# Kernel tuning notes

Hardware: AMD Instinct MI355X
Metric: run time of the kernel (lower is better)

## Reference

```python
import jax, jax.numpy as jnp
import numpy as np


def setup_inputs() -> dict:
    key = jax.random.key(0)
    ks = jax.random.split(key, 10)
    B, T = 64, 2048
    inp_p, inp_q, out = 512, 512, 512
    def xavier(k, shape):
        fan_in, fan_out = shape[1], shape[0]
        limit = np.sqrt(6.0 / (fan_in + fan_out))
        return jax.random.uniform(k, shape, jnp.float32, -limit, limit)
    return {
        "input_p": jax.random.normal(ks[0], (B, inp_p), jnp.float32),
        "input_q": jax.random.normal(ks[1], (B, T, inp_q), jnp.float32),
        "h_tm1": jax.random.normal(ks[2], (B, out), jnp.float32),
        "Wp": xavier(ks[3], (out, inp_p)),
        "bp": jnp.zeros((out,), jnp.float32),
        "Wq": xavier(ks[4], (out, inp_q)),
        "bq": jnp.zeros((out,), jnp.float32),
        "Wr": xavier(ks[5], (out, out)),
        "br": jnp.zeros((out,), jnp.float32),
        "w": 0.05 * jax.random.normal(ks[6], (out,), jnp.float32),
        "match_b": jnp.ones((1,), jnp.float32),
        "depth": 0,
    }


def reference(input_p, input_q, h_tm1, Wp, bp, Wq, bq, Wr, br, w, match_b, depth):
    # depth selects the layer; single layer (depth=0) parameters provided.
    G_p = (input_p @ Wp.T + bp)[:, None, :]          # [B, 1, out]
    G_q = jnp.einsum("btq,oq->bto", input_q, Wq) + bq  # [B, T, out]
    G_r = (h_tm1 @ Wr.T + br)[:, None, :]            # [B, 1, out]
    G = jnp.tanh(G_p + G_q + G_r)                    # [B, T, out]
    alpha = jnp.einsum("bto,o->bt", G, w) + match_b[0]  # [B, T]
    alpha = jax.nn.softmax(alpha, axis=-1)
    z = jnp.einsum("bt,btq->bq", alpha, input_q)     # [B, inp_q]
    return jnp.concatenate([input_p, z], axis=1)     # [B, inp_p+inp_q]
```

## Files before the change

### kernel.cpp

```cpp
#include <hip/hip_runtime.h>
#include <stdint.h>
#include <stddef.h>


typedef __attribute__((ext_vector_type(8))) short short8;
typedef __attribute__((ext_vector_type(8))) unsigned short ushort8v;
typedef __attribute__((ext_vector_type(4))) float f32x4;

__device__ __forceinline__ unsigned short f2bf(float f) {
    unsigned int u = __builtin_bit_cast(unsigned int, f);
    return (unsigned short)((u + 0x7FFFu + ((u >> 16) & 1u)) >> 16);
}

__device__ __forceinline__ void gload_lds16(const void* g, void* l) {
    __builtin_amdgcn_global_load_lds(
        (const __attribute__((address_space(1))) unsigned int*)g,
        (__attribute__((address_space(3))) unsigned int*)l, 16, 0, 0);
}

__global__ __launch_bounds__(256) void k_zero(float* __restrict__ p) {
    int i = (blockIdx.x * 256 + threadIdx.x) * 4;
    *(float4*)(p + i) = make_float4(0.f, 0.f, 0.f, 0.f);
}

__global__ __launch_bounds__(256) void k_convert(const float* __restrict__ Wq,
                                                 unsigned short* __restrict__ Wq_bf) {
    int i = (blockIdx.x * 256 + threadIdx.x) * 8;
    float4 a = *(const float4*)(Wq + i);
    float4 b = *(const float4*)(Wq + i + 4);
    ushort8v o;
    o[0] = f2bf(a.x); o[1] = f2bf(a.y); o[2] = f2bf(a.z); o[3] = f2bf(a.w);
    o[4] = f2bf(b.x); o[5] = f2bf(b.y); o[6] = f2bf(b.z); o[7] = f2bf(b.w);
    *(ushort8v*)(Wq_bf + i) = o;
}

__global__ __launch_bounds__(256) void k_prq(
        const float* __restrict__ ip, const float* __restrict__ h,
        const float* __restrict__ Wp, const float* __restrict__ Wr,
        const float* __restrict__ bp, const float* __restrict__ bq,
        const float* __restrict__ br, float* __restrict__ prq) {
    __shared__ float ip_lds[64][68];
    __shared__ float h_lds[64][68];
    __shared__ float wp_lds[8][68];
    __shared__ float wr_lds[8][68];
    const int tid = threadIdx.x;
    const int o0 = blockIdx.x * 8;
    const int bb = tid >> 3;
    const int oo = tid & 7;
    float acc0 = 0.f, acc1 = 0.f;
    const int lrow = tid >> 2;
    const int lcol = (tid & 3) * 16;
    for (int kc = 0; kc < 512; kc += 64) {
        #pragma unroll
        for (int j = 0; j < 16; j += 4) {
            float4 v = *(const float4*)(ip + lrow * 512 + kc + lcol + j);
            ip_lds[lrow][lcol + j] = v.x; ip_lds[lrow][lcol + j + 1] = v.y;
            ip_lds[lrow][lcol + j + 2] = v.z; ip_lds[lrow][lcol + j + 3] = v.w;
            float4 u = *(const float4*)(h + lrow * 512 + kc + lcol + j);
            h_lds[lrow][lcol + j] = u.x; h_lds[lrow][lcol + j + 1] = u.y;
            h_lds[lrow][lcol + j + 2] = u.z; h_lds[lrow][lcol + j + 3] = u.w;
        }
        if (tid < 128) {
            int r = tid >> 4, c = (tid & 15) * 4;
            float4 v = *(const float4*)(Wp + (size_t)(o0 + r) * 512 + kc + c);
            wp_lds[r][c] = v.x; wp_lds[r][c + 1] = v.y; wp_lds[r][c + 2] = v.z; wp_lds[r][c + 3] = v.w;
        } else {
            int t2 = tid - 128;
            int r = t2 >> 4, c = (t2 & 15) * 4;
            float4 v = *(const float4*)(Wr + (size_t)(o0 + r) * 512 + kc + c);
            wr_lds[r][c] = v.x; wr_lds[r][c + 1] = v.y; wr_lds[r][c + 2] = v.z; wr_lds[r][c + 3] = v.w;
        }
        __syncthreads();
        #pragma unroll 4
        for (int k = 0; k < 64; ++k) {
            float wpv = wp_lds[oo][k], wrv = wr_lds[oo][k];
            acc0 += ip_lds[bb][k] * wpv + h_lds[bb][k] * wrv;
            acc1 += ip_lds[bb + 32][k] * wpv + h_lds[bb + 32][k] * wrv;
        }
        __syncthreads();
    }
    const int o = o0 + oo;
    float base = bp[o] + bq[o] + br[o];
    prq[bb * 512 + o] = acc0 + base;
    prq[(bb + 32) * 512 + o] = acc1 + base;
}

__global__ __launch_bounds__(256, 3) void k_gq(
        const float* __restrict__ iq, const unsigned short* __restrict__ Wq_bf,
        const float* __restrict__ prq, const float* __restrict__ wv,
        float* __restrict__ logits) {
    __shared__ float A_t[128][32];
    __shared__ unsigned short B_t[128][32];
    __shared__ float w_lds[128];
    __shared__ float prq_lds[128];
    __shared__ float red[2][128];

    const int tid = threadIdx.x;
    const int bid = blockIdx.x;
    const int orig = (bid & 7) * 512 + (bid >> 3);
    const int m0 = (orig >> 2) * 128;
    const int n0 = (orig & 3) * 128;
    const int b = m0 >> 11;

    if (tid < 128) {
        w_lds[tid] = wv[n0 + tid];
        prq_lds[tid] = prq[b * 512 + n0 + tid];
    }

    const int lane = tid & 63;
    const int wave = tid >> 6;
    const int wm = wave >> 1;
    const int wn = wave & 1;
    const int r16 = lane & 15;
    const int cc = lane >> 4;

    const int ha0 = (((2 * cc) ^ (r16 & 7)) << 2);
    const int ha1 = (((2 * cc + 1) ^ (r16 & 7)) << 2);
    const int bswz = ((cc ^ ((r16 >> 1) & 3)) << 3);

    const float* asrc[4];
    #pragma unroll
    for (int r = 0; r < 4; ++r) {
        int t = r * 256 + tid;
        int row = t >> 3, s = t & 7;
        asrc[r] = iq + (size_t)(m0 + row) * 512 + ((s ^ (row & 7)) << 2);
    }
    const unsigned short* bsrc[2];
    #pragma unroll
    for (int r = 0; r < 2; ++r) {
        int u = r * 256 + tid;
        int row = u >> 2, s = u & 3;
        bsrc[r] = Wq_bf + (size_t)(n0 + row) * 512 + ((s ^ ((row >> 1) & 3)) << 3);
    }
    char* adst = (char*)A_t + wave * 1024;
    char* bdst = (char*)B_t + wave * 1024;

    f32x4 acc[4][4];
    #pragma unroll
    for (int i = 0; i < 4; ++i)
        #pragma unroll
        for (int j = 0; j < 4; ++j) acc[i][j] = (f32x4){0.f, 0.f, 0.f, 0.f};

    for (int k0 = 0; k0 < 512; k0 += 32) {
        gload_lds16(asrc[0] + k0, adst);
        gload_lds16(asrc[1] + k0, adst + 4096);
        gload_lds16(asrc[2] + k0, adst + 8192);
        gload_lds16(asrc[3] + k0, adst + 12288);
        gload_lds16(bsrc[0] + k0, bdst);
        gload_lds16(bsrc[1] + k0, bdst + 4096);
        __syncthreads();

        short8 af[4];
        #pragma unroll
        for (int mf = 0; mf < 4; ++mf) {
            const float* rp = &A_t[wm * 64 + mf * 16 + r16][0];
            f32x4 x0 = *(const f32x4*)(rp + ha0);
            f32x4 x1 = *(const f32x4*)(rp + ha1);
            ushort8v u;
            u[0] = f2bf(x0[0]); u[1] = f2bf(x0[1]); u[2] = f2bf(x0[2]); u[3] = f2bf(x0[3]);
            u[4] = f2bf(x1[0]); u[5] = f2bf(x1[1]); u[6] = f2bf(x1[2]); u[7] = f2bf(x1[3]);
            af[mf] = __builtin_bit_cast(short8, u);
        }
        #pragma unroll
        for (int nf = 0; nf < 4; ++nf) {
            short8 bfr = *(const short8*)&B_t[wn * 64 + nf * 16 + r16][bswz];
            #pragma unroll
            for (int mf = 0; mf < 4; ++mf)
                acc[mf][nf] = __builtin_amdgcn_mfma_f32_16x16x32_bf16(af[mf], bfr, acc[mf][nf], 0, 0, 0);
        }
        __syncthreads();
    }

    float part[4][4];
    #pragma unroll
    for (int mf = 0; mf < 4; ++mf)
        #pragma unroll
        for (int j = 0; j < 4; ++j) part[mf][j] = 0.f;

    #pragma unroll
    for (int nf = 0; nf < 4; ++nf) {
        int c = wn * 64 + nf * 16 + r16;
        float wc = w_lds[c];
        float pc = prq_lds[c];
        #pragma unroll
        for (int mf = 0; mf < 4; ++mf) {
            #pragma unroll
            for (int j = 0; j < 4; ++j) {
                float x = acc[mf][nf][j] + pc;
                float e = __expf(2.f * x);
                part[mf][j] += wc * (1.f - 2.f / (e + 1.f));
            }
        }
    }
    #pragma unroll
    for (int mf = 0; mf < 4; ++mf)
        #pragma unroll
        for (int j = 0; j < 4; ++j) {
            float v = part[mf][j];
            v += __shfl_xor(v, 1);
            v += __shfl_xor(v, 2);
            v += __shfl_xor(v, 4);
            v += __shfl_xor(v, 8);
            part[mf][j] = v;
        }
    if (r16 == 0) {
        #pragma unroll
        for (int mf = 0; mf < 4; ++mf)
            #pragma unroll
            for (int j = 0; j < 4; ++j)
                red[wn][wm * 64 + mf * 16 + cc * 4 + j] = part[mf][j];
    }
    __syncthreads();
    if (tid < 128)
        atomicAdd(&logits[m0 + tid], red[0][tid] + red[1][tid]);
}

__global__ __launch_bounds__(256) void k_stats(const float* __restrict__ logits,
                                               const float* __restrict__ ip,
                                               float* __restrict__ out,
                                               float* __restrict__ stats) {
    const int b = blockIdx.x, tid = threadIdx.x;
    __shared__ float sm[256];
    float m = -1e30f;
    for (int i = tid; i < 2048; i += 256) m = fmaxf(m, logits[b * 2048 + i]);
    sm[tid] = m;
    __syncthreads();
    for (int s = 128; s > 0; s >>= 1) {
        if (tid < s) sm[tid] = fmaxf(sm[tid], sm[tid + s]);
        __syncthreads();
    }
    float bmax = sm[0];
    __syncthreads();
    float ssum = 0.f;
    for (int i = tid; i < 2048; i += 256) ssum += __expf(logits[b * 2048 + i] - bmax);
    sm[tid] = ssum;
    __syncthreads();
    for (int s = 128; s > 0; s >>= 1) {
        if (tid < s) sm[tid] += sm[tid + s];
        __syncthreads();
    }
    if (tid == 0) { stats[b * 2] = bmax; stats[b * 2 + 1] = sm[0]; }
    out[b * 1024 + tid] = ip[b * 512 + tid];
    out[b * 1024 + 256 + tid] = ip[b * 512 + 256 + tid];
    out[b * 1024 + 512 + tid] = 0.f;
    out[b * 1024 + 768 + tid] = 0.f;
}

#define TC 128
__global__ __launch_bounds__(256) void k_z(const float* __restrict__ logits,
                                           const float* __restrict__ stats,
                                           const float* __restrict__ iq,
                                           float* __restrict__ out) {
    const int blk = blockIdx.x;
    const int b = blk >> 4;
    const int c = blk & 15;
    const int tid = threadIdx.x;
    __shared__ float al[TC];
    const float bmax = stats[b * 2];
    const float inv = 1.f / stats[b * 2 + 1];
    if (tid < TC) al[tid] = __expf(logits[b * 2048 + c * TC + tid] - bmax) * inv;
    __syncthreads();
    const int q = tid * 2;
    float ax = 0.f, ay = 0.f;
    const float* base = iq + ((size_t)b * 2048 + (size_t)c * TC) * 512 + q;
    #pragma unroll 4
    for (int t = 0; t < TC; ++t) {
        float2 v = *(const float2*)(base + (size_t)t * 512);
        float a = al[t];
        ax += a * v.x;
        ay += a * v.y;
    }
    atomicAdd(&out[b * 1024 + 512 + q], ax);
    atomicAdd(&out[b * 1024 + 512 + q + 1], ay);
}

extern "C" void kernel_launch(void* const* d_in, const int* in_sizes, int n_in,
                              void* d_out, int out_size, void* d_ws, size_t ws_size,
                              hipStream_t stream) {
    const float* input_p = (const float*)d_in[0];
    const float* input_q = (const float*)d_in[1];
    const float* h_tm1   = (const float*)d_in[2];
    const float* Wp      = (const float*)d_in[3];
    const float* bp      = (const float*)d_in[4];
    const float* Wq      = (const float*)d_in[5];
    const float* bq      = (const float*)d_in[6];
    const float* Wr      = (const float*)d_in[7];
    const float* br      = (const float*)d_in[8];
    const float* wv      = (const float*)d_in[9];
    float* out = (float*)d_out;

    char* ws = (char*)d_ws;
    unsigned short* Wq_bf = (unsigned short*)ws;
    float* prq    = (float*)(ws + 512 * 1024);
    float* logits = (float*)(ws + 640 * 1024);
    float* stats  = (float*)(ws + 1152 * 1024);

    k_zero<<<dim3(128), dim3(256), 0, stream>>>(logits);
    k_convert<<<dim3(128), dim3(256), 0, stream>>>(Wq, Wq_bf);
    k_prq<<<dim3(64), dim3(256), 0, stream>>>(input_p, h_tm1, Wp, Wr, bp, bq, br, prq);
    k_gq<<<dim3(4096), dim3(256), 0, stream>>>(input_q, Wq_bf, prq, wv, logits);
    k_stats<<<dim3(64), dim3(256), 0, stream>>>(logits, input_p, out, stats);
    k_z<<<dim3(64 * 16), dim3(256), 0, stream>>>(logits, stats, input_q, out);
}
```

Baseline: 219.0 us.

## Prefetch fp32 A tile into registers and store bf16 to LDS

```diff
diff --git a/kernel.cpp b/kernel.cpp
--- a/kernel.cpp
+++ b/kernel.cpp
@@ -1,4 +1,5 @@
 #include <hip/hip_runtime.h>
+#include <hip/hip_bf16.h>
 #include <stdint.h>
 #include <stddef.h>
 
@@ -89,7 +90,7 @@
         const float* __restrict__ iq, const unsigned short* __restrict__ Wq_bf,
         const float* __restrict__ prq, const float* __restrict__ wv,
         float* __restrict__ logits) {
-    __shared__ float A_t[128][32];
+    __shared__ unsigned short A_t[128][32];
     __shared__ unsigned short B_t[128][32];
     __shared__ float w_lds[128];
     __shared__ float prq_lds[128];
@@ -113,18 +114,18 @@
     const int wn = wave & 1;
     const int r16 = lane & 15;
     const int cc = lane >> 4;
-
-    const int ha0 = (((2 * cc) ^ (r16 & 7)) << 2);
-    const int ha1 = (((2 * cc + 1) ^ (r16 & 7)) << 2);
-    const int bswz = ((cc ^ ((r16 >> 1) & 3)) << 3);
-
+    const int swz = ((cc ^ ((r16 >> 1) & 3)) << 3);
+
+    const int g4 = tid & 7;
     const float* asrc[4];
+    unsigned short* adst[4];
     #pragma unroll
     for (int r = 0; r < 4; ++r) {
-        int t = r * 256 + tid;
-        int row = t >> 3, s = t & 7;
-        asrc[r] = iq + (size_t)(m0 + row) * 512 + ((s ^ (row & 7)) << 2);
-    }
+        int arow = r * 32 + (tid >> 3);
+        asrc[r] = iq + (size_t)(m0 + arow) * 512 + g4 * 4;
+        adst[r] = &A_t[arow][(((g4 >> 1) ^ ((arow >> 1) & 3)) << 3) + (g4 & 1) * 4];
+    }
+
     const unsigned short* bsrc[2];
     #pragma unroll
     for (int r = 0; r < 2; ++r) {
@@ -132,7 +133,6 @@
         int row = u >> 2, s = u & 3;
         bsrc[r] = Wq_bf + (size_t)(n0 + row) * 512 + ((s ^ ((row >> 1) & 3)) << 3);
     }
-    char* adst = (char*)A_t + wave * 1024;
     char* bdst = (char*)B_t + wave * 1024;
 
     f32x4 acc[4][4];
@@ -141,35 +141,53 @@
         #pragma unroll
         for (int j = 0; j < 4; ++j) acc[i][j] = (f32x4){0.f, 0.f, 0.f, 0.f};
 
-    for (int k0 = 0; k0 < 512; k0 += 32) {
-        gload_lds16(asrc[0] + k0, adst);
-        gload_lds16(asrc[1] + k0, adst + 4096);
-        gload_lds16(asrc[2] + k0, adst + 8192);
-        gload_lds16(asrc[3] + k0, adst + 12288);
-        gload_lds16(bsrc[0] + k0, bdst);
-        gload_lds16(bsrc[1] + k0, bdst + 4096);
-        __syncthreads();
-
-        short8 af[4];
-        #pragma unroll
-        for (int mf = 0; mf < 4; ++mf) {
-            const float* rp = &A_t[wm * 64 + mf * 16 + r16][0];
-            f32x4 x0 = *(const f32x4*)(rp + ha0);
-            f32x4 x1 = *(const f32x4*)(rp + ha1);
-            ushort8v u;
-            u[0] = f2bf(x0[0]); u[1] = f2bf(x0[1]); u[2] = f2bf(x0[2]); u[3] = f2bf(x0[3]);
-            u[4] = f2bf(x1[0]); u[5] = f2bf(x1[1]); u[6] = f2bf(x1[2]); u[7] = f2bf(x1[3]);
-            af[mf] = __builtin_bit_cast(short8, u);
-        }
-        #pragma unroll
-        for (int nf = 0; nf < 4; ++nf) {
-            short8 bfr = *(const short8*)&B_t[wn * 64 + nf * 16 + r16][bswz];
-            #pragma unroll
-            for (int mf = 0; mf < 4; ++mf)
-                acc[mf][nf] = __builtin_amdgcn_mfma_f32_16x16x32_bf16(af[mf], bfr, acc[mf][nf], 0, 0, 0);
-        }
-        __syncthreads();
-    }
+    float4 rA[4], rB[4];
+
+#define LOADA(RN, K)                                   \
+    RN[0] = *(const float4*)(asrc[0] + (K));           \
+    RN[1] = *(const float4*)(asrc[1] + (K));           \
+    RN[2] = *(const float4*)(asrc[2] + (K));           \
+    RN[3] = *(const float4*)(asrc[3] + (K));
+
+#define CVTW(RC, r)                                                              \
+    {                                                                            \
+        union { __hip_bfloat162 h[2]; uint2 v; } u_;                             \
+        u_.h[0] = __float22bfloat162_rn(make_float2(RC[r].x, RC[r].y));          \
+        u_.h[1] = __float22bfloat162_rn(make_float2(RC[r].z, RC[r].w));          \
+        *(uint2*)adst[r] = u_.v;                                                 \
+    }
+
+#define STEP(K0, RC, RN, KN)                                                     \
+    {                                                                            \
+        __syncthreads();                                                         \
+        CVTW(RC, 0) CVTW(RC, 1) CVTW(RC, 2) CVTW(RC, 3)                          \
+        gload_lds16(bsrc[0] + (K0), bdst);                                       \
+        gload_lds16(bsrc[1] + (K0), bdst + 4096);                                \
+        __syncthreads();                                                         \
+        LOADA(RN, KN);                                                           \
+        short8 af[4];                                                            \
+        af[0] = *(const short8*)&A_t[wm * 64 + 0 * 16 + r16][swz];               \
+        af[1] = *(const short8*)&A_t[wm * 64 + 1 * 16 + r16][swz];               \
+        af[2] = *(const short8*)&A_t[wm * 64 + 2 * 16 + r16][swz];               \
+        af[3] = *(const short8*)&A_t[wm * 64 + 3 * 16 + r16][swz];               \
+        _Pragma("unroll")                                                        \
+        for (int nf = 0; nf < 4; ++nf) {                                         \
+            short8 bfr = *(const short8*)&B_t[wn * 64 + nf * 16 + r16][swz];     \
+            acc[0][nf] = __builtin_amdgcn_mfma_f32_16x16x32_bf16(af[0], bfr, acc[0][nf], 0, 0, 0); \
+            acc[1][nf] = __builtin_amdgcn_mfma_f32_16x16x32_bf16(af[1], bfr, acc[1][nf], 0, 0, 0); \
+            acc[2][nf] = __builtin_amdgcn_mfma_f32_16x16x32_bf16(af[2], bfr, acc[2][nf], 0, 0, 0); \
+            acc[3][nf] = __builtin_amdgcn_mfma_f32_16x16x32_bf16(af[3], bfr, acc[3][nf], 0, 0, 0); \
+        }                                                                        \
+    }
+
+    LOADA(rA, 0);
+    for (int k0 = 0; k0 < 512; k0 += 64) {
+        STEP(k0, rA, rB, k0 + 32);
+        STEP(k0 + 32, rB, rA, (k0 + 64 < 512) ? (k0 + 64) : 480);
+    }
+#undef STEP
+#undef CVTW
+#undef LOADA
 
     float part[4][4];
     #pragma unroll
```

Result: slower. 226.3 us (+3.4%).

## Double-buffer GEMM tiles and convert A to bf16 once during staging

Applied to the files above, without the earlier changes.

```diff
diff --git a/kernel.cpp b/kernel.cpp
--- a/kernel.cpp
+++ b/kernel.cpp
@@ -1,4 +1,5 @@
 #include <hip/hip_runtime.h>
+#include <hip/hip_bf16.h>
 #include <stdint.h>
 #include <stddef.h>
 
@@ -16,6 +17,15 @@
     __builtin_amdgcn_global_load_lds(
         (const __attribute__((address_space(1))) unsigned int*)g,
         (__attribute__((address_space(3))) unsigned int*)l, 16, 0, 0);
+}
+
+__device__ __forceinline__ short8 cvt8(float4 a, float4 b) {
+    union { __hip_bfloat162 h[4]; short8 s; } u;
+    u.h[0] = __float22bfloat162_rn(make_float2(a.x, a.y));
+    u.h[1] = __float22bfloat162_rn(make_float2(a.z, a.w));
+    u.h[2] = __float22bfloat162_rn(make_float2(b.x, b.y));
+    u.h[3] = __float22bfloat162_rn(make_float2(b.z, b.w));
+    return u.s;
 }
 
 __global__ __launch_bounds__(256) void k_zero(float* __restrict__ p) {
@@ -89,8 +99,8 @@
         const float* __restrict__ iq, const unsigned short* __restrict__ Wq_bf,
         const float* __restrict__ prq, const float* __restrict__ wv,
         float* __restrict__ logits) {
-    __shared__ float A_t[128][32];
-    __shared__ unsigned short B_t[128][32];
+    __shared__ unsigned short A2[2][4096];
+    __shared__ unsigned short B2[2][4096];
     __shared__ float w_lds[128];
     __shared__ float prq_lds[128];
     __shared__ float red[2][128];
@@ -113,27 +123,20 @@
     const int wn = wave & 1;
     const int r16 = lane & 15;
     const int cc = lane >> 4;
-
-    const int ha0 = (((2 * cc) ^ (r16 & 7)) << 2);
-    const int ha1 = (((2 * cc + 1) ^ (r16 & 7)) << 2);
-    const int bswz = ((cc ^ ((r16 >> 1) & 3)) << 3);
-
-    const float* asrc[4];
-    #pragma unroll
-    for (int r = 0; r < 4; ++r) {
-        int t = r * 256 + tid;
-        int row = t >> 3, s = t & 7;
-        asrc[r] = iq + (size_t)(m0 + row) * 512 + ((s ^ (row & 7)) << 2);
-    }
-    const unsigned short* bsrc[2];
-    #pragma unroll
-    for (int r = 0; r < 2; ++r) {
-        int u = r * 256 + tid;
-        int row = u >> 2, s = u & 3;
-        bsrc[r] = Wq_bf + (size_t)(n0 + row) * 512 + ((s ^ ((row >> 1) & 3)) << 3);
-    }
-    char* adst = (char*)A_t + wave * 1024;
-    char* bdst = (char*)B_t + wave * 1024;
+    const int swz = ((cc ^ ((r16 >> 1) & 3)) << 3);
+
+    const int ar0 = tid >> 2, ac0 = tid & 3;
+    const int ar1 = 64 + (tid >> 2), ac1 = tid & 3;
+    const float* asrc0 = iq + (size_t)(m0 + ar0) * 512 + ac0 * 8;
+    const float* asrc1 = iq + (size_t)(m0 + ar1) * 512 + ac1 * 8;
+    const int aoff0 = ar0 * 32 + ((ac0 ^ ((ar0 >> 1) & 3)) << 3);
+    const int aoff1 = ar1 * 32 + ((ac1 ^ ((ar1 >> 1) & 3)) << 3);
+
+    const int brw0 = tid >> 2, bs0 = (tid & 3) ^ ((brw0 >> 1) & 3);
+    const int brw1 = 64 + (tid >> 2);
+    const int bs1 = (tid & 3) ^ ((brw1 >> 1) & 3);
+    const unsigned short* bsrc0 = Wq_bf + (size_t)(n0 + brw0) * 512 + (bs0 << 3);
+    const unsigned short* bsrc1 = Wq_bf + (size_t)(n0 + brw1) * 512 + (bs1 << 3);
 
     f32x4 acc[4][4];
     #pragma unroll
@@ -141,35 +144,56 @@
         #pragma unroll
         for (int j = 0; j < 4; ++j) acc[i][j] = (f32x4){0.f, 0.f, 0.f, 0.f};
 
-    for (int k0 = 0; k0 < 512; k0 += 32) {
-        gload_lds16(asrc[0] + k0, adst);
-        gload_lds16(asrc[1] + k0, adst + 4096);
-        gload_lds16(asrc[2] + k0, adst + 8192);
-        gload_lds16(asrc[3] + k0, adst + 12288);
-        gload_lds16(bsrc[0] + k0, bdst);
-        gload_lds16(bsrc[1] + k0, bdst + 4096);
-        __syncthreads();
-
-        short8 af[4];
-        #pragma unroll
-        for (int mf = 0; mf < 4; ++mf) {
-            const float* rp = &A_t[wm * 64 + mf * 16 + r16][0];
-            f32x4 x0 = *(const f32x4*)(rp + ha0);
-            f32x4 x1 = *(const f32x4*)(rp + ha1);
-            ushort8v u;
-            u[0] = f2bf(x0[0]); u[1] = f2bf(x0[1]); u[2] = f2bf(x0[2]); u[3] = f2bf(x0[3]);
-            u[4] = f2bf(x1[0]); u[5] = f2bf(x1[1]); u[6] = f2bf(x1[2]); u[7] = f2bf(x1[3]);
-            af[mf] = __builtin_bit_cast(short8, u);
-        }
-        #pragma unroll
-        for (int nf = 0; nf < 4; ++nf) {
-            short8 bfr = *(const short8*)&B_t[wn * 64 + nf * 16 + r16][bswz];
-            #pragma unroll
-            for (int mf = 0; mf < 4; ++mf)
-                acc[mf][nf] = __builtin_amdgcn_mfma_f32_16x16x32_bf16(af[mf], bfr, acc[mf][nf], 0, 0, 0);
-        }
-        __syncthreads();
-    }
+    float4 ra0, ra1, ra2, ra3;
+
+    gload_lds16(bsrc0, (char*)&B2[0][0] + wave * 1024);
+    gload_lds16(bsrc1, (char*)&B2[0][0] + 4096 + wave * 1024);
+    ra0 = *(const float4*)(asrc0);
+    ra1 = *(const float4*)(asrc0 + 4);
+    ra2 = *(const float4*)(asrc1);
+    ra3 = *(const float4*)(asrc1 + 4);
+    *(short8*)&A2[0][aoff0] = cvt8(ra0, ra1);
+    *(short8*)&A2[0][aoff1] = cvt8(ra2, ra3);
+    asm volatile("s_waitcnt vmcnt(0) lgkmcnt(0)" ::: "memory");
+    __builtin_amdgcn_sched_barrier(0);
+    __builtin_amdgcn_s_barrier();
+
+#define PHASE(K, C, PF)                                                          \
+    {                                                                            \
+        if (PF) {                                                                \
+            gload_lds16(bsrc0 + (K) + 32, (char*)&B2[(C) ^ 1][0] + wave * 1024); \
+            gload_lds16(bsrc1 + (K) + 32, (char*)&B2[(C) ^ 1][0] + 4096 + wave * 1024); \
+            ra0 = *(const float4*)(asrc0 + (K) + 32);                            \
+            ra1 = *(const float4*)(asrc0 + (K) + 36);                            \
+            ra2 = *(const float4*)(asrc1 + (K) + 32);                            \
+            ra3 = *(const float4*)(asrc1 + (K) + 36);                            \
+        }                                                                        \
+        short8 af0 = *(const short8*)&A2[C][(wm * 64 +  0 + r16) * 32 + swz];    \
+        short8 af1 = *(const short8*)&A2[C][(wm * 64 + 16 + r16) * 32 + swz];    \
+        short8 af2 = *(const short8*)&A2[C][(wm * 64 + 32 + r16) * 32 + swz];    \
+        short8 af3 = *(const short8*)&A2[C][(wm * 64 + 48 + r16) * 32 + swz];    \
+        _Pragma("unroll")                                                        \
+        for (int nf = 0; nf < 4; ++nf) {                                         \
+            short8 bfr = *(const short8*)&B2[C][(wn * 64 + nf * 16 + r16) * 32 + swz]; \
+            acc[0][nf] = __builtin_amdgcn_mfma_f32_16x16x32_bf16(af0, bfr, acc[0][nf], 0, 0, 0); \
+            acc[1][nf] = __builtin_amdgcn_mfma_f32_16x16x32_bf16(af1, bfr, acc[1][nf], 0, 0, 0); \
+            acc[2][nf] = __builtin_amdgcn_mfma_f32_16x16x32_bf16(af2, bfr, acc[2][nf], 0, 0, 0); \
+            acc[3][nf] = __builtin_amdgcn_mfma_f32_16x16x32_bf16(af3, bfr, acc[3][nf], 0, 0, 0); \
+        }                                                                        \
+        if (PF) {                                                                \
+            *(short8*)&A2[(C) ^ 1][aoff0] = cvt8(ra0, ra1);                      \
+            *(short8*)&A2[(C) ^ 1][aoff1] = cvt8(ra2, ra3);                      \
+        }                                                                        \
+        asm volatile("s_waitcnt vmcnt(0) lgkmcnt(0)" ::: "memory");              \
+        __builtin_amdgcn_sched_barrier(0);                                       \
+        __builtin_amdgcn_s_barrier();                                            \
+    }
+
+    for (int kk = 0; kk < 512; kk += 64) {
+        PHASE(kk, 0, 1);
+        PHASE(kk + 32, 1, (kk + 64) < 512);
+    }
+#undef PHASE
 
     float part[4][4];
     #pragma unroll
```

Result: faster. 205.8 us (-6.0%).
